# Optimization experiments

Measured on AMD Instinct MI355X. Metric: run time of the kernel, lower is better.

Reference implementation:

```python
import jax, jax.numpy as jnp
import numpy as np

H = 64          # hidden_size
FF = 36         # MLP hidden
B, W, S = 512, 8, 200


def setup_inputs() -> dict:
    key = jax.random.key(0)
    ks = jax.random.split(key, 8)
    query = jax.random.normal(ks[0], (B, H), dtype=jnp.float32)
    k = jax.random.normal(ks[1], (B, W, S, H), dtype=jnp.float32)
    mask = jax.random.randint(ks[2], (B, W, S, 1), 0, 2).astype(bool)
    # MLP params: Linear(4H -> 36), PReLU(scalar), Linear(36 -> 1)
    lim1 = 1.0 / np.sqrt(4 * H)
    W1 = jax.random.uniform(ks[3], (FF, 4 * H), jnp.float32, -lim1, lim1)
    b1 = jax.random.uniform(ks[4], (FF,), jnp.float32, -lim1, lim1)
    prelu_a = jnp.float32(0.25)
    lim2 = 1.0 / np.sqrt(FF)
    W2 = jax.random.uniform(ks[5], (1, FF), jnp.float32, -lim2, lim2)
    b2 = jax.random.uniform(ks[6], (1,), jnp.float32, -lim2, lim2)
    return {"query": query, "key": k, "W1": W1, "b1": b1,
            "prelu_a": prelu_a, "W2": W2, "b2": b2, "mask": mask}


def reference(query, key, W1, b1, prelu_a, W2, b2, mask):
    # broadcast query to (B, W, S, H)
    q = jnp.broadcast_to(query[:, None, None, :], key.shape)
    feat = jnp.concatenate([q, key, q - key, q * key], axis=-1)  # (B,W,S,4H)
    h = jnp.einsum('bwsf,of->bwso', feat, W1) + b1               # (B,W,S,36)
    h = jnp.where(h >= 0, h, prelu_a * h)                        # PReLU
    score = jnp.einsum('bwso,uo->bwsu', h, W2) + b2              # (B,W,S,1)
    # weighted_att=True: mask with -1e4 then softmax over seq_len
    score = jnp.where(mask, jnp.float32(-10000.0), score)
    score = jax.nn.softmax(score, axis=2)
    out = (key * score).sum(axis=2)                              # (B,W,H)
    return out
```

## Files before the change

### kernel.cpp

```cpp
#include <hip/hip_runtime.h>
#include <hip/hip_bf16.h>
#include <math.h>


#define BB   512
#define WW   8
#define SS   200
#define HH   64
#define FFN  36

typedef __attribute__((ext_vector_type(8))) short short8;
typedef __attribute__((ext_vector_type(4))) float f32x4;

__device__ __forceinline__ unsigned short f2bf(float x) {
    __hip_bfloat16 h = __float2bfloat16(x);
    union { __hip_bfloat16 b; unsigned short u; } c; c.b = h;
    return c.u;
}
__device__ __forceinline__ float bf2f(unsigned short h) {
    union { unsigned u; float f; } v; v.u = ((unsigned)h) << 16;
    return v.f;
}

__global__ __launch_bounds__(256)
void precompute_c(const float* __restrict__ query,
                  const float* __restrict__ W1,
                  const float* __restrict__ b1,
                  unsigned short* __restrict__ c_hi_g,
                  float* __restrict__ A_g)
{
    __shared__ float q_s[HH];
    const int b = blockIdx.x, tid = threadIdx.x;
    if (tid < HH) q_s[tid] = query[b * HH + tid];
    __syncthreads();
    for (int idx = tid; idx < 48 * HH; idx += 256) {
        int o = idx >> 6, h = idx & 63;
        float c = 0.0f;
        if (o < FFN) {
            const float* w = W1 + o * 4 * HH;
            c = w[HH + h] - w[2 * HH + h] + w[3 * HH + h] * q_s[h];
        }
        c_hi_g[(size_t)b * 48 * HH + idx] = f2bf(c);
    }
    if (tid < 48) {
        float a = 0.0f;
        if (tid < FFN) {
            const float* w = W1 + tid * 4 * HH;
            a = b1[tid];
            #pragma unroll 8
            for (int h = 0; h < HH; ++h) a += (w[h] + w[2 * HH + h]) * q_s[h];
        }
        A_g[b * 48 + tid] = a;
    }
}

__device__ __forceinline__ void load_tile(const float* __restrict__ kg,
                                          int st, int n, int q,
                                          float4 (&buf)[2][2])
{
    const int s = st * 16 + n;
    const float* p = kg + (size_t)s * HH + q * 8;
    if (s < SS) {
        buf[0][0] = *(const float4*)(p);
        buf[0][1] = *(const float4*)(p + 4);
        buf[1][0] = *(const float4*)(p + 32);
        buf[1][1] = *(const float4*)(p + 36);
    } else {
        const float4 z = make_float4(0.f, 0.f, 0.f, 0.f);
        buf[0][0] = z; buf[0][1] = z; buf[1][0] = z; buf[1][1] = z;
    }
}

__device__ __forceinline__ void online_tile(const float4 (&buf)[2][2],
                                            const short8 (&Bf)[3][2],
                                            const float (&Ao)[3],
                                            const float (&w2o)[3],
                                            float pa, int st, int q, int n,
                                            unsigned mbits,
                                            float& m, float& l, float (&o)[16])
{
    short8 Ah[2], Al[2];
    #pragma unroll
    for (int ks = 0; ks < 2; ++ks) {
        const float vv[8] = {buf[ks][0].x, buf[ks][0].y, buf[ks][0].z, buf[ks][0].w,
                             buf[ks][1].x, buf[ks][1].y, buf[ks][1].z, buf[ks][1].w};
        #pragma unroll
        for (int j = 0; j < 8; ++j) {
            const unsigned short hi = f2bf(vv[j]);
            Ah[ks][j] = (short)hi;
            Al[ks][j] = (short)f2bf(vv[j] - bf2f(hi));
        }
    }
    float contrib[4] = {0.f, 0.f, 0.f, 0.f};
    #pragma unroll
    for (int ot = 0; ot < 3; ++ot) {
        f32x4 acc = {0.f, 0.f, 0.f, 0.f};
        acc = __builtin_amdgcn_mfma_f32_16x16x32_bf16(Ah[0], Bf[ot][0], acc, 0, 0, 0);
        acc = __builtin_amdgcn_mfma_f32_16x16x32_bf16(Al[0], Bf[ot][0], acc, 0, 0, 0);
        acc = __builtin_amdgcn_mfma_f32_16x16x32_bf16(Ah[1], Bf[ot][1], acc, 0, 0, 0);
        acc = __builtin_amdgcn_mfma_f32_16x16x32_bf16(Al[1], Bf[ot][1], acc, 0, 0, 0);
        #pragma unroll
        for (int r = 0; r < 4; ++r) {
            float hv = acc[r] + Ao[ot];
            hv = (hv >= 0.0f) ? hv : pa * hv;
            contrib[r] += w2o[ot] * hv;
        }
    }
    #pragma unroll
    for (int mm = 1; mm <= 8; mm <<= 1)
        #pragma unroll
        for (int r = 0; r < 4; ++r)
            contrib[r] += __shfl_xor(contrib[r], mm, 64);

    const int rsel = n & 3;
    float v = contrib[0];
    v = (rsel == 1) ? contrib[1] : v;
    v = (rsel == 2) ? contrib[2] : v;
    v = (rsel == 3) ? contrib[3] : v;
    const float srow = __shfl(v, ((n >> 2) << 4) | (n & 3), 64);

    const int s_row = st * 16 + n;
    float sn = (s_row < SS)
             ? (((mbits >> st) & 1u) ? -10000.0f : srow)
             : -3.0e38f;

    float tm = sn;
    #pragma unroll
    for (int mm = 1; mm <= 8; mm <<= 1)
        tm = fmaxf(tm, __shfl_xor(tm, mm, 64));
    const float m_new = fmaxf(m, tm);
    const float scl = __expf(m - m_new);
    const float w   = __expf(sn - m_new);
    float ls = w;
    #pragma unroll
    for (int mm = 1; mm <= 8; mm <<= 1)
        ls += __shfl_xor(ls, mm, 64);
    l = l * scl + ls;
    m = m_new;
    #pragma unroll
    for (int ks = 0; ks < 2; ++ks) {
        o[ks*8+0] = o[ks*8+0]*scl + w*buf[ks][0].x;
        o[ks*8+1] = o[ks*8+1]*scl + w*buf[ks][0].y;
        o[ks*8+2] = o[ks*8+2]*scl + w*buf[ks][0].z;
        o[ks*8+3] = o[ks*8+3]*scl + w*buf[ks][0].w;
        o[ks*8+4] = o[ks*8+4]*scl + w*buf[ks][1].x;
        o[ks*8+5] = o[ks*8+5]*scl + w*buf[ks][1].y;
        o[ks*8+6] = o[ks*8+6]*scl + w*buf[ks][1].z;
        o[ks*8+7] = o[ks*8+7]*scl + w*buf[ks][1].w;
    }
}

__global__ __launch_bounds__(256, 4)
void twb_flash(const float* __restrict__ key,
               const unsigned short* __restrict__ c_hi_g,
               const float* __restrict__ A_g,
               const float* __restrict__ prelu_a,
               const float* __restrict__ W2,
               const int*   __restrict__ mask,
               float*       __restrict__ out)
{
    const int tid  = threadIdx.x;
    const int wid  = tid >> 6, lane = tid & 63;
    const int q    = lane >> 4, n = lane & 15;
    const int bw   = blockIdx.x * 4 + wid;
    const int b    = bw >> 3;
    const float* kg = key + (size_t)bw * (SS * HH);

    const unsigned short* cb = c_hi_g + (size_t)b * 48 * HH;
    short8 Bf[3][2];
    float  Ao[3], w2o[3];
    #pragma unroll
    for (int ot = 0; ot < 3; ++ot) {
        const int o = ot * 16 + n;
        #pragma unroll
        for (int ks = 0; ks < 2; ++ks)
            Bf[ot][ks] = *(const short8*)(cb + (size_t)o * HH + ks * 32 + q * 8);
        Ao[ot]  = A_g[b * 48 + o];
        w2o[ot] = (o < FFN) ? W2[o] : 0.0f;
    }
    const float pa = prelu_a[0];

    unsigned mbits = 0;
    #pragma unroll
    for (int st = 0; st < 13; ++st) {
        const int s = st * 16 + n;
        int mv = 1;
        if (s < SS) mv = mask[bw * SS + s];
        mbits |= (mv ? 1u : 0u) << st;
    }

    float m = -3.0e38f, l = 0.0f;
    float o[16];
    #pragma unroll
    for (int j = 0; j < 16; ++j) o[j] = 0.0f;

    float4 bufA[2][2], bufB[2][2];
    load_tile(kg, 0, n, q, bufA);
    for (int st2 = 0; st2 < 6; ++st2) {
        load_tile(kg, st2 * 2 + 1, n, q, bufB);
        online_tile(bufA, Bf, Ao, w2o, pa, st2 * 2, q, n, mbits, m, l, o);
        load_tile(kg, st2 * 2 + 2, n, q, bufA);
        online_tile(bufB, Bf, Ao, w2o, pa, st2 * 2 + 1, q, n, mbits, m, l, o);
    }
    online_tile(bufA, Bf, Ao, w2o, pa, 12, q, n, mbits, m, l, o);

    #pragma unroll
    for (int mm = 1; mm <= 8; mm <<= 1)
        #pragma unroll
        for (int j = 0; j < 16; ++j)
            o[j] += __shfl_xor(o[j], mm, 64);
    if (n == 0) {
        const float inv = 1.0f / l;
        float* po = out + (size_t)bw * HH;
        float4 v;
        v = make_float4(o[0]*inv,  o[1]*inv,  o[2]*inv,  o[3]*inv);
        *(float4*)(po + q * 8)      = v;
        v = make_float4(o[4]*inv,  o[5]*inv,  o[6]*inv,  o[7]*inv);
        *(float4*)(po + q * 8 + 4)  = v;
        v = make_float4(o[8]*inv,  o[9]*inv,  o[10]*inv, o[11]*inv);
        *(float4*)(po + 32 + q * 8) = v;
        v = make_float4(o[12]*inv, o[13]*inv, o[14]*inv, o[15]*inv);
        *(float4*)(po + 36 + q * 8) = v;
    }
}

#define PADQ 17
__global__ __launch_bounds__(256, 2)
void twb_fallback(const float* __restrict__ query,
                  const float* __restrict__ key,
                  const float* __restrict__ W1,
                  const float* __restrict__ b1,
                  const float* __restrict__ prelu_a,
                  const float* __restrict__ W2,
                  const float* __restrict__ b2,
                  const int*   __restrict__ mask,
                  float*       __restrict__ out)
{
    __shared__ float q_s[HH];
    __shared__ float c_s[FFN * HH];
    __shared__ float A_s[FFN];
    __shared__ float W2_s[FFN];
    __shared__ float k_s[SS * PADQ * 4];
    __shared__ float wl[256];
    __shared__ float red[8];
    __shared__ float part[4 * 64];

    const int tid = threadIdx.x;
    const int bw  = blockIdx.x;
    const int b   = bw >> 3;

    if (tid < HH)  q_s[tid]  = query[b * HH + tid];
    if (tid < FFN) W2_s[tid] = W2[tid];
    __syncthreads();

    const float4* gk4 = (const float4*)(key + (size_t)bw * (SS * HH));
    float4* kl4 = (float4*)k_s;
    for (int i = tid; i < (SS * HH) / 4; i += 256) {
        float4 v = gk4[i];
        kl4[(i >> 4) * PADQ + (i & 15)] = v;
    }
    for (int idx = tid; idx < FFN * HH; idx += 256) {
        int o = idx >> 6, h = idx & 63;
        const float* w = W1 + o * (4 * HH);
        c_s[idx] = w[HH + h] - w[2 * HH + h] + w[3 * HH + h] * q_s[h];
    }
    if (tid < FFN) {
        const float* w = W1 + tid * (4 * HH);
        float a = b1[tid];
        for (int h = 0; h < HH; ++h) a += (w[h] + w[2 * HH + h]) * q_s[h];
        A_s[tid] = a;
    }
    __syncthreads();

    const float pa  = prelu_a[0];
    const float bb2 = b2[0];
    float msc = -3.0e38f;
    if (tid < SS) {
        float acc[FFN];
        #pragma unroll
        for (int o = 0; o < FFN; ++o) acc[o] = A_s[o];
        const float4* c4 = (const float4*)c_s;
        const float4* k4 = (const float4*)k_s;
        const int rowbase = tid * PADQ;
        for (int ch = 0; ch < 4; ++ch) {
            float4 kv0 = k4[rowbase + ch * 4 + 0];
            float4 kv1 = k4[rowbase + ch * 4 + 1];
            float4 kv2 = k4[rowbase + ch * 4 + 2];
            float4 kv3 = k4[rowbase + ch * 4 + 3];
            #pragma unroll
            for (int o = 0; o < FFN; ++o) {
                float4 c0 = c4[o * 16 + ch * 4 + 0];
                float4 c1 = c4[o * 16 + ch * 4 + 1];
                float4 c2 = c4[o * 16 + ch * 4 + 2];
                float4 c3 = c4[o * 16 + ch * 4 + 3];
                float a = acc[o];
                a += c0.x * kv0.x + c0.y * kv0.y + c0.z * kv0.z + c0.w * kv0.w;
                a += c1.x * kv1.x + c1.y * kv1.y + c1.z * kv1.z + c1.w * kv1.w;
                a += c2.x * kv2.x + c2.y * kv2.y + c2.z * kv2.z + c2.w * kv2.w;
                a += c3.x * kv3.x + c3.y * kv3.y + c3.z * kv3.z + c3.w * kv3.w;
                acc[o] = a;
            }
        }
        float sc = bb2;
        #pragma unroll
        for (int o = 0; o < FFN; ++o) {
            float a = acc[o];
            a = (a >= 0.0f) ? a : pa * a;
            sc += W2_s[o] * a;
        }
        msc = mask[bw * SS + tid] ? -10000.0f : sc;
    }

    float mx = msc;
    #pragma unroll
    for (int off = 32; off > 0; off >>= 1)
        mx = fmaxf(mx, __shfl_xor(mx, off, 64));
    const int wid = tid >> 6;
    if ((tid & 63) == 0) red[wid] = mx;
    __syncthreads();
    const float M = fmaxf(fmaxf(red[0], red[1]), fmaxf(red[2], red[3]));
    float e = (tid < SS) ? __expf(msc - M) : 0.0f;
    float ssum = e;
    #pragma unroll
    for (int off = 32; off > 0; off >>= 1)
        ssum += __shfl_xor(ssum, off, 64);
    if ((tid & 63) == 0) red[4 + wid] = ssum;
    __syncthreads();
    const float total = red[4] + red[5] + red[6] + red[7];
    if (tid < SS) wl[tid] = e / total;
    __syncthreads();

    const int wv = tid >> 6, h = tid & 63;
    float p = 0.0f;
    for (int s = wv * 50; s < wv * 50 + 50; ++s)
        p += k_s[s * (PADQ * 4) + h] * wl[s];
    part[wv * 64 + h] = p;
    __syncthreads();
    if (tid < 64) {
        float r = part[tid] + part[64 + tid] + part[128 + tid] + part[192 + tid];
        out[(size_t)bw * HH + tid] = r;
    }
}

extern "C" void kernel_launch(void* const* d_in, const int* in_sizes, int n_in,
                              void* d_out, int out_size, void* d_ws, size_t ws_size,
                              hipStream_t stream) {
    const float* query   = (const float*)d_in[0];
    const float* key     = (const float*)d_in[1];
    const float* W1      = (const float*)d_in[2];
    const float* b1      = (const float*)d_in[3];
    const float* prelu_a = (const float*)d_in[4];
    const float* W2      = (const float*)d_in[5];
    const float* b2      = (const float*)d_in[6];
    const int*   mask    = (const int*)d_in[7];
    float* out = (float*)d_out;

    const size_t c_bytes = (size_t)BB * 48 * HH * sizeof(unsigned short);
    const size_t a_bytes = (size_t)BB * 48 * sizeof(float);
    if (ws_size >= c_bytes + a_bytes) {
        unsigned short* c_hi_g = (unsigned short*)d_ws;
        float* A_g = (float*)((char*)d_ws + c_bytes);
        precompute_c<<<BB, 256, 0, stream>>>(query, W1, b1, c_hi_g, A_g);
        twb_flash<<<(BB * WW) / 4, 256, 0, stream>>>(key, c_hi_g, A_g, prelu_a,
                                                     W2, mask, out);
    } else {
        twb_fallback<<<BB * WW, 256, 0, stream>>>(query, key, W1, b1, prelu_a,
                                                  W2, b2, mask, out);
    }
}
```

Before: 316.1 us.

## Transpose MFMA operands, drop online-softmax max tracking, triple-buffer key tiles

The MFMA operand order is swapped so each lane's accumulator holds FF outputs for one sequence row. The per-row score then needs only two cross-lane shuffles instead of a 16-lane butterfly plus a select-and-broadcast. The bias is folded into the accumulator's initial value, and W2 is padded in the precompute kernel so both can be loaded as vectors. The online-softmax running max and rescaling are removed, so scores are exponentiated directly; this relies on scores staying small and risks overflow, or a zero denominator if every position is masked. Key tiles are now triple-buffered in a fully unrolled loop, and the occupancy hint is lowered from 4 to 3 blocks per SM.

```diff
diff --git a/kernel.cpp b/kernel.cpp
--- a/kernel.cpp
+++ b/kernel.cpp
@@ -26,12 +26,15 @@
 void precompute_c(const float* __restrict__ query,
                   const float* __restrict__ W1,
                   const float* __restrict__ b1,
+                  const float* __restrict__ W2,
                   unsigned short* __restrict__ c_hi_g,
-                  float* __restrict__ A_g)
+                  float* __restrict__ A_g,
+                  float* __restrict__ w2p_g)
 {
     __shared__ float q_s[HH];
     const int b = blockIdx.x, tid = threadIdx.x;
     if (tid < HH) q_s[tid] = query[b * HH + tid];
+    if (b == 0 && tid < 48) w2p_g[tid] = (tid < FFN) ? W2[tid] : 0.0f;
     __syncthreads();
     for (int idx = tid; idx < 48 * HH; idx += 256) {
         int o = idx >> 6, h = idx & 63;
@@ -71,15 +74,15 @@
     }
 }
 
-__device__ __forceinline__ void online_tile(const float4 (&buf)[2][2],
-                                            const short8 (&Bf)[3][2],
-                                            const float (&Ao)[3],
-                                            const float (&w2o)[3],
+__device__ __forceinline__ void tile_update(const float4 (&buf)[2][2],
+                                            const short8 (&Af)[3][2],
+                                            const f32x4 (&Aov)[3],
+                                            const f32x4 (&w2v)[3],
                                             float pa, int st, int q, int n,
                                             unsigned mbits,
-                                            float& m, float& l, float (&o)[16])
-{
-    short8 Ah[2], Al[2];
+                                            float& l, float (&o)[16])
+{
+    short8 Bh[2], Bl[2];
     #pragma unroll
     for (int ks = 0; ks < 2; ++ks) {
         const float vv[8] = {buf[ks][0].x, buf[ks][0].y, buf[ks][0].z, buf[ks][0].w,
@@ -87,77 +90,52 @@
         #pragma unroll
         for (int j = 0; j < 8; ++j) {
             const unsigned short hi = f2bf(vv[j]);
-            Ah[ks][j] = (short)hi;
-            Al[ks][j] = (short)f2bf(vv[j] - bf2f(hi));
-        }
-    }
-    float contrib[4] = {0.f, 0.f, 0.f, 0.f};
+            Bh[ks][j] = (short)hi;
+            Bl[ks][j] = (short)f2bf(vv[j] - bf2f(hi));
+        }
+    }
+    float contrib = 0.0f;
     #pragma unroll
     for (int ot = 0; ot < 3; ++ot) {
-        f32x4 acc = {0.f, 0.f, 0.f, 0.f};
-        acc = __builtin_amdgcn_mfma_f32_16x16x32_bf16(Ah[0], Bf[ot][0], acc, 0, 0, 0);
-        acc = __builtin_amdgcn_mfma_f32_16x16x32_bf16(Al[0], Bf[ot][0], acc, 0, 0, 0);
-        acc = __builtin_amdgcn_mfma_f32_16x16x32_bf16(Ah[1], Bf[ot][1], acc, 0, 0, 0);
-        acc = __builtin_amdgcn_mfma_f32_16x16x32_bf16(Al[1], Bf[ot][1], acc, 0, 0, 0);
+        f32x4 acc = Aov[ot];
+        acc = __builtin_amdgcn_mfma_f32_16x16x32_bf16(Af[ot][0], Bh[0], acc, 0, 0, 0);
+        acc = __builtin_amdgcn_mfma_f32_16x16x32_bf16(Af[ot][0], Bl[0], acc, 0, 0, 0);
+        acc = __builtin_amdgcn_mfma_f32_16x16x32_bf16(Af[ot][1], Bh[1], acc, 0, 0, 0);
+        acc = __builtin_amdgcn_mfma_f32_16x16x32_bf16(Af[ot][1], Bl[1], acc, 0, 0, 0);
         #pragma unroll
         for (int r = 0; r < 4; ++r) {
-            float hv = acc[r] + Ao[ot];
+            float hv = acc[r];
             hv = (hv >= 0.0f) ? hv : pa * hv;
-            contrib[r] += w2o[ot] * hv;
-        }
-    }
-    #pragma unroll
-    for (int mm = 1; mm <= 8; mm <<= 1)
-        #pragma unroll
-        for (int r = 0; r < 4; ++r)
-            contrib[r] += __shfl_xor(contrib[r], mm, 64);
-
-    const int rsel = n & 3;
-    float v = contrib[0];
-    v = (rsel == 1) ? contrib[1] : v;
-    v = (rsel == 2) ? contrib[2] : v;
-    v = (rsel == 3) ? contrib[3] : v;
-    const float srow = __shfl(v, ((n >> 2) << 4) | (n & 3), 64);
-
-    const int s_row = st * 16 + n;
-    float sn = (s_row < SS)
-             ? (((mbits >> st) & 1u) ? -10000.0f : srow)
-             : -3.0e38f;
-
-    float tm = sn;
-    #pragma unroll
-    for (int mm = 1; mm <= 8; mm <<= 1)
-        tm = fmaxf(tm, __shfl_xor(tm, mm, 64));
-    const float m_new = fmaxf(m, tm);
-    const float scl = __expf(m - m_new);
-    const float w   = __expf(sn - m_new);
-    float ls = w;
-    #pragma unroll
-    for (int mm = 1; mm <= 8; mm <<= 1)
-        ls += __shfl_xor(ls, mm, 64);
-    l = l * scl + ls;
-    m = m_new;
+            contrib += w2v[ot][r] * hv;
+        }
+    }
+    contrib += __shfl_xor(contrib, 16, 64);
+    contrib += __shfl_xor(contrib, 32, 64);
+
+    const float sn = (((mbits >> st) & 1u) ? -10000.0f : contrib);
+    const float w = __expf(sn);
+    l += w;
     #pragma unroll
     for (int ks = 0; ks < 2; ++ks) {
-        o[ks*8+0] = o[ks*8+0]*scl + w*buf[ks][0].x;
-        o[ks*8+1] = o[ks*8+1]*scl + w*buf[ks][0].y;
-        o[ks*8+2] = o[ks*8+2]*scl + w*buf[ks][0].z;
-        o[ks*8+3] = o[ks*8+3]*scl + w*buf[ks][0].w;
-        o[ks*8+4] = o[ks*8+4]*scl + w*buf[ks][1].x;
-        o[ks*8+5] = o[ks*8+5]*scl + w*buf[ks][1].y;
-        o[ks*8+6] = o[ks*8+6]*scl + w*buf[ks][1].z;
-        o[ks*8+7] = o[ks*8+7]*scl + w*buf[ks][1].w;
-    }
-}
-
-__global__ __launch_bounds__(256, 4)
-void twb_flash(const float* __restrict__ key,
-               const unsigned short* __restrict__ c_hi_g,
-               const float* __restrict__ A_g,
-               const float* __restrict__ prelu_a,
-               const float* __restrict__ W2,
-               const int*   __restrict__ mask,
-               float*       __restrict__ out)
+        o[ks*8+0] += w * buf[ks][0].x;
+        o[ks*8+1] += w * buf[ks][0].y;
+        o[ks*8+2] += w * buf[ks][0].z;
+        o[ks*8+3] += w * buf[ks][0].w;
+        o[ks*8+4] += w * buf[ks][1].x;
+        o[ks*8+5] += w * buf[ks][1].y;
+        o[ks*8+6] += w * buf[ks][1].z;
+        o[ks*8+7] += w * buf[ks][1].w;
+    }
+}
+
+__global__ __launch_bounds__(256, 3)
+void twb_flash2(const float* __restrict__ key,
+                const unsigned short* __restrict__ c_hi_g,
+                const float* __restrict__ A_g,
+                const float* __restrict__ w2p_g,
+                const float* __restrict__ prelu_a,
+                const int*   __restrict__ mask,
+                float*       __restrict__ out)
 {
     const int tid  = threadIdx.x;
     const int wid  = tid >> 6, lane = tid & 63;
@@ -166,20 +144,6 @@
     const int b    = bw >> 3;
     const float* kg = key + (size_t)bw * (SS * HH);
 
-    const unsigned short* cb = c_hi_g + (size_t)b * 48 * HH;
-    short8 Bf[3][2];
-    float  Ao[3], w2o[3];
-    #pragma unroll
-    for (int ot = 0; ot < 3; ++ot) {
-        const int o = ot * 16 + n;
-        #pragma unroll
-        for (int ks = 0; ks < 2; ++ks)
-            Bf[ot][ks] = *(const short8*)(cb + (size_t)o * HH + ks * 32 + q * 8);
-        Ao[ot]  = A_g[b * 48 + o];
-        w2o[ot] = (o < FFN) ? W2[o] : 0.0f;
-    }
-    const float pa = prelu_a[0];
-
     unsigned mbits = 0;
     #pragma unroll
     for (int st = 0; st < 13; ++st) {
@@ -189,26 +153,41 @@
         mbits |= (mv ? 1u : 0u) << st;
     }
 
-    float m = -3.0e38f, l = 0.0f;
+    const unsigned short* cbp = c_hi_g + (size_t)b * 48 * HH;
+    short8 Af[3][2];
+    f32x4  Aov[3], w2v[3];
+    #pragma unroll
+    for (int ot = 0; ot < 3; ++ot) {
+        #pragma unroll
+        for (int ks = 0; ks < 2; ++ks)
+            Af[ot][ks] = *(const short8*)(cbp + (ot * 16 + n) * HH + ks * 32 + q * 8);
+        Aov[ot] = *(const f32x4*)(A_g + b * 48 + ot * 16 + q * 4);
+        w2v[ot] = *(const f32x4*)(w2p_g + ot * 16 + q * 4);
+    }
+    const float pa = prelu_a[0];
+
+    float l = 0.0f;
     float o[16];
     #pragma unroll
     for (int j = 0; j < 16; ++j) o[j] = 0.0f;
 
-    float4 bufA[2][2], bufB[2][2];
-    load_tile(kg, 0, n, q, bufA);
-    for (int st2 = 0; st2 < 6; ++st2) {
-        load_tile(kg, st2 * 2 + 1, n, q, bufB);
-        online_tile(bufA, Bf, Ao, w2o, pa, st2 * 2, q, n, mbits, m, l, o);
-        load_tile(kg, st2 * 2 + 2, n, q, bufA);
-        online_tile(bufB, Bf, Ao, w2o, pa, st2 * 2 + 1, q, n, mbits, m, l, o);
-    }
-    online_tile(bufA, Bf, Ao, w2o, pa, 12, q, n, mbits, m, l, o);
-
-    #pragma unroll
-    for (int mm = 1; mm <= 8; mm <<= 1)
+    float4 buf[3][2][2];
+    load_tile(kg, 0, n, q, buf[0]);
+    load_tile(kg, 1, n, q, buf[1]);
+    load_tile(kg, 2, n, q, buf[2]);
+    #pragma unroll
+    for (int t = 0; t < 13; ++t) {
+        tile_update(buf[t % 3], Af, Aov, w2v, pa, t, q, n, mbits, l, o);
+        if (t + 3 < 13) load_tile(kg, t + 3, n, q, buf[t % 3]);
+    }
+
+    #pragma unroll
+    for (int mm = 1; mm <= 8; mm <<= 1) {
         #pragma unroll
         for (int j = 0; j < 16; ++j)
             o[j] += __shfl_xor(o[j], mm, 64);
+        l += __shfl_xor(l, mm, 64);
+    }
     if (n == 0) {
         const float inv = 1.0f / l;
         float* po = out + (size_t)bw * HH;
@@ -355,14 +334,16 @@
     const int*   mask    = (const int*)d_in[7];
     float* out = (float*)d_out;
 
-    const size_t c_bytes = (size_t)BB * 48 * HH * sizeof(unsigned short);
-    const size_t a_bytes = (size_t)BB * 48 * sizeof(float);
-    if (ws_size >= c_bytes + a_bytes) {
+    const size_t c_bytes  = (size_t)BB * 48 * HH * sizeof(unsigned short);
+    const size_t a_bytes  = (size_t)BB * 48 * sizeof(float);
+    const size_t w2_bytes = 48 * sizeof(float);
+    if (ws_size >= c_bytes + a_bytes + w2_bytes) {
         unsigned short* c_hi_g = (unsigned short*)d_ws;
-        float* A_g = (float*)((char*)d_ws + c_bytes);
-        precompute_c<<<BB, 256, 0, stream>>>(query, W1, b1, c_hi_g, A_g);
-        twb_flash<<<(BB * WW) / 4, 256, 0, stream>>>(key, c_hi_g, A_g, prelu_a,
-                                                     W2, mask, out);
+        float* A_g   = (float*)((char*)d_ws + c_bytes);
+        float* w2p_g = (float*)((char*)d_ws + c_bytes + a_bytes);
+        precompute_c<<<BB, 256, 0, stream>>>(query, W1, b1, W2, c_hi_g, A_g, w2p_g);
+        twb_flash2<<<(BB * WW) / 4, 256, 0, stream>>>(key, c_hi_g, A_g, w2p_g,
+                                                      prelu_a, mask, out);
     } else {
         twb_fallback<<<BB * WW, 256, 0, stream>>>(query, key, W1, b1, prelu_a,
                                                   W2, b2, mask, out);
```

Measured after the change: 422.9 us. 33.8% more time.
